# Kernel optimization log

Measured on AMD Instinct MI355X. Metric: run time of the kernel, lower is better.

## Reference

```python
import jax, jax.numpy as jnp
import numpy as np

H = 1024          # hidden_size
NH = 16           # num_attention_heads
HD = H // NH      # attention_head_size = 64
B, S = 8, 1024
LN_EPS = 1e-12


def setup_inputs() -> dict:
    key = jax.random.key(0)
    ks = jax.random.split(key, 12)
    sc = 0.02
    return {
        "input_tensor": jax.random.normal(ks[0], (B, S, H), dtype=jnp.float32),
        "attention_mask": jnp.zeros((B, S), dtype=jnp.float32),
        # LinearMem params (quantization disabled -> plain Linear, torch layout [out,in])
        "Wq": jax.random.normal(ks[1], (H, H), dtype=jnp.float32) * sc,
        "bq": jnp.zeros((H,), dtype=jnp.float32),
        "Wk": jax.random.normal(ks[2], (H, H), dtype=jnp.float32) * sc,
        "bk": jnp.zeros((H,), dtype=jnp.float32),
        "Wv": jax.random.normal(ks[3], (H, H), dtype=jnp.float32) * sc,
        "bv": jnp.zeros((H,), dtype=jnp.float32),
        "Wo": jax.random.normal(ks[4], (H, H), dtype=jnp.float32) * sc,
        "bo": jnp.zeros((H,), dtype=jnp.float32),
        "ln_gamma": jnp.ones((H,), dtype=jnp.float32),
        "ln_beta": jnp.zeros((H,), dtype=jnp.float32),
    }


def _heads(x):  # [B,S,H] -> [B,NH,S,HD]
    return x.reshape(B, S, NH, HD).transpose(0, 2, 1, 3)


def reference(input_tensor, attention_mask, Wq, bq, Wk, bk, Wv, bv, Wo, bo, ln_gamma, ln_beta):
    # Q/K/V projections (LinearMem with quantization disabled == Linear)
    q = _heads(jnp.einsum('bsh,oh->bso', input_tensor, Wq) + bq)
    k = _heads(jnp.einsum('bsh,oh->bso', input_tensor, Wk) + bk)
    v = _heads(jnp.einsum('bsh,oh->bso', input_tensor, Wv) + bv)
    scores = jnp.einsum('bnqd,bnkd->bnqk', q, k) / np.float32(np.sqrt(HD))
    scores = scores + attention_mask[:, None, None, :]  # additive mask [B,1,1,S]
    probs = jax.nn.softmax(scores, axis=-1)  # dropout = identity in eval
    ctx = jnp.einsum('bnqk,bnkd->bnqd', probs, v)
    ctx = ctx.transpose(0, 2, 1, 3).reshape(B, S, H)
    # output projection + residual LayerNorm (eps=1e-12)
    out = jnp.einsum('bsh,oh->bso', ctx, Wo) + bo
    resid = out + input_tensor
    mu = jnp.mean(resid, axis=-1, keepdims=True)
    var = jnp.mean(jnp.square(resid - mu), axis=-1, keepdims=True)
    return (resid - mu) * jax.lax.rsqrt(var + LN_EPS) * ln_gamma + ln_beta
```

## Files before the change

### kernel.cpp

```cpp
#include <hip/hip_runtime.h>

#define NHh 16

typedef unsigned short ushortT;
typedef __attribute__((ext_vector_type(8))) short short8;
typedef __attribute__((ext_vector_type(4))) float floatx4;

__device__ __forceinline__ ushortT f2bf(float x) {
    union { float f; unsigned int u; } cv; cv.f = x;
    unsigned int u = cv.u;
    unsigned int r = u + 0x7fffu + ((u >> 16) & 1u);
    return (ushortT)(r >> 16);
}

__device__ __forceinline__ unsigned pack2_trunc(float a, float b) {
    union { float f; unsigned u; } ua, ub;
    ua.f = a; ub.f = b;
    return (ub.u & 0xffff0000u) | (ua.u >> 16);
}

__device__ __forceinline__ void gload_lds16(const ushortT* g, ushortT* l) {
    __builtin_amdgcn_global_load_lds(
        (const __attribute__((address_space(1))) void*)g,
        (__attribute__((address_space(3))) void*)l, 16, 0, 0);
}

__global__ __launch_bounds__(256) void cvt_x(const float* __restrict__ in,
                                             ushortT* __restrict__ out, int n4) {
    int i = blockIdx.x * 256 + threadIdx.x;
    if (i >= n4) return;
    float4 f = ((const float4*)in)[i];
    uint2 o;
    o.x = (unsigned)f2bf(f.x) | ((unsigned)f2bf(f.y) << 16);
    o.y = (unsigned)f2bf(f.z) | ((unsigned)f2bf(f.w) << 16);
    ((uint2*)out)[i] = o;
}

__global__ __launch_bounds__(256) void cvt_w(const float* __restrict__ W0, const float* __restrict__ W1,
                                             const float* __restrict__ W2, const float* __restrict__ W3,
                                             ushortT* __restrict__ Wall, ushortT* __restrict__ Wob, int n4) {
    int z = blockIdx.y;
    const float* in = (z == 0) ? W0 : (z == 1) ? W1 : (z == 2) ? W2 : W3;
    ushortT* out = (z < 3) ? (Wall + (size_t)z * 1048576) : Wob;
    int i = blockIdx.x * 256 + threadIdx.x;
    if (i >= n4) return;
    float4 f = ((const float4*)in)[i];
    uint2 o;
    o.x = (unsigned)f2bf(f.x) | ((unsigned)f2bf(f.y) << 16);
    o.y = (unsigned)f2bf(f.z) | ((unsigned)f2bf(f.w) << 16);
    ((uint2*)out)[i] = o;
}

__global__ __launch_bounds__(512, 1) void qkv_st(
        const ushortT* __restrict__ X, const ushortT* __restrict__ Wall,
        const float* __restrict__ b0, const float* __restrict__ b1, const float* __restrict__ b2,
        ushortT* __restrict__ Qo, ushortT* __restrict__ Ko, ushortT* __restrict__ Vo) {
    __shared__ __align__(16) ushortT As[2 * 16384];
    __shared__ __align__(16) ushortT Bs[2 * 12288];

    const int l = blockIdx.x;
    const int xcd = l & 7;
    const int j = l >> 3;
    const int mg = j >> 4;
    const int nt = j & 15;
    const int arow0 = (mg * 8 + xcd) * 256;
    const int brow0 = nt * 192;

    const int tid = threadIdx.x;
    const int lane = tid & 63;
    const int w = tid >> 6;
    const int wr = w >> 2;
    const int wc = w & 3;
    const int qd = lane >> 4, ln = lane & 15;

    const ushortT* srcA[4]; const ushortT* srcB[3];
    int oA[4], oB[3];
#pragma unroll
    for (int k = 0; k < 4; k++) {
        int o = k * 8192 + tid * 16;
        int rowblk = o >> 11, ks = (o >> 10) & 1, r = (o >> 6) & 15;
        int c2 = ((o >> 4) & 3) ^ ((r >> 3) << 1);
        srcA[k] = X + (size_t)(arow0 + rowblk * 16 + r) * 1024 + ks * 32 + c2 * 8;
        oA[k] = o;
    }
#pragma unroll
    for (int k = 0; k < 3; k++) {
        int o = k * 8192 + tid * 16;
        int rowblk = o >> 11, ks = (o >> 10) & 1, r = (o >> 6) & 15;
        int c2 = ((o >> 4) & 3) ^ ((r >> 3) << 1);
        srcB[k] = Wall + (size_t)(brow0 + rowblk * 16 + r) * 1024 + ks * 32 + c2 * 8;
        oB[k] = o;
    }

    floatx4 acc[8][3];
#pragma unroll
    for (int i = 0; i < 8; i++)
#pragma unroll
        for (int jj = 0; jj < 3; jj++) acc[i][jj] = (floatx4){0.f, 0.f, 0.f, 0.f};

#pragma unroll
    for (int k = 0; k < 4; k++) { gload_lds16(srcA[k], As + oA[k] / 2); srcA[k] += 64; }
#pragma unroll
    for (int k = 0; k < 3; k++) { gload_lds16(srcB[k], Bs + oB[k] / 2); srcB[k] += 64; }
    asm volatile("s_waitcnt vmcnt(0)" ::: "memory");
    __builtin_amdgcn_s_barrier();

    const int lnc = ln * 64 + ((qd ^ ((ln >> 3) << 1)) * 16);

    for (int T = 0; T < 16; T++) {
        const char* Ab = (const char*)As + (T & 1) * 32768;
        const char* Bb = (const char*)Bs + (T & 1) * 24576;
        short8 afr[8][2], bfr[3][2];
#pragma unroll
        for (int mi = 0; mi < 8; mi++)
#pragma unroll
            for (int ks = 0; ks < 2; ks++)
                afr[mi][ks] = *(const short8*)(Ab + (wr * 8 + mi) * 2048 + ks * 1024 + lnc);
#pragma unroll
        for (int ni = 0; ni < 3; ni++)
#pragma unroll
            for (int ks = 0; ks < 2; ks++)
                bfr[ni][ks] = *(const short8*)(Bb + (wc * 3 + ni) * 2048 + ks * 1024 + lnc);
        if (T < 15) {
            char* An = (char*)As + ((T + 1) & 1) * 32768;
            char* Bn = (char*)Bs + ((T + 1) & 1) * 24576;
#pragma unroll
            for (int k = 0; k < 4; k++) { gload_lds16(srcA[k], (ushortT*)(An + oA[k])); srcA[k] += 64; }
#pragma unroll
            for (int k = 0; k < 3; k++) { gload_lds16(srcB[k], (ushortT*)(Bn + oB[k])); srcB[k] += 64; }
        }
        __builtin_amdgcn_s_barrier();
        asm volatile("s_waitcnt lgkmcnt(0)" ::: "memory");
        __builtin_amdgcn_sched_barrier(0);
        __builtin_amdgcn_s_setprio(1);
#pragma unroll
        for (int mi = 0; mi < 8; mi++)
#pragma unroll
            for (int ni = 0; ni < 3; ni++)
#pragma unroll
                for (int ks = 0; ks < 2; ks++)
                    acc[mi][ni] = __builtin_amdgcn_mfma_f32_16x16x32_bf16(
                        afr[mi][ks], bfr[ni][ks], acc[mi][ni], 0, 0, 0);
        __builtin_amdgcn_s_setprio(0);
        asm volatile("s_waitcnt vmcnt(0)" ::: "memory");
        __builtin_amdgcn_s_barrier();
    }

#pragma unroll
    for (int ni = 0; ni < 3; ni++) {
        int n = brow0 + wc * 48 + ni * 16 + ln;
        int z = n >> 10;
        int col = n & 1023;
        int h = col >> 6, d = col & 63;
        const float* bias = (z == 0) ? b0 : (z == 1) ? b1 : b2;
        float bb = bias[col];
        if (z == 2) {
#pragma unroll
            for (int mi = 0; mi < 8; mi++) {
                int m = arow0 + wr * 128 + mi * 16 + qd * 4;
                int b = m >> 10, s = m & 1023;
                ushort4 pk;
                pk.x = f2bf(acc[mi][ni][0] + bb);
                pk.y = f2bf(acc[mi][ni][1] + bb);
                pk.z = f2bf(acc[mi][ni][2] + bb);
                pk.w = f2bf(acc[mi][ni][3] + bb);
                *(ushort4*)&Vo[((size_t)(b * NHh + h) * 64 + d) * 1024 + s] = pk;
            }
        } else {
            ushortT* Out = z ? Ko : Qo;
#pragma unroll
            for (int mi = 0; mi < 8; mi++) {
#pragma unroll
                for (int r2 = 0; r2 < 4; r2++) {
                    int m = arow0 + wr * 128 + mi * 16 + qd * 4 + r2;
                    int b = m >> 10, s = m & 1023;
                    Out[(size_t)((b * NHh + h) * 1024 + s) * 64 + d] =
                        f2bf(acc[mi][ni][r2] + bb);
                }
            }
        }
    }
}

__device__ __forceinline__ void gemm_core_256x128(
        const ushortT* __restrict__ Ap, const ushortT* __restrict__ Bp,
        int arow0, int brow0, ushortT* As3, ushortT* Bs3,
        int tid, int wr, int wc, int qd, int ln, floatx4 (&acc)[4][4]) {
    const ushortT* srcA[4]; const ushortT* srcB[2];
    int oA[4], oB[2];
#pragma unroll
    for (int k = 0; k < 4; k++) {
        int o = k * 8192 + tid * 16;
        int rowblk = o >> 11, ks = (o >> 10) & 1, r = (o >> 6) & 15;
        int c2 = ((o >> 4) & 3) ^ ((r >> 3) << 1);
        srcA[k] = Ap + (size_t)(arow0 + rowblk * 16 + r) * 1024 + ks * 32 + c2 * 8;
        oA[k] = o;
    }
#pragma unroll
    for (int k = 0; k < 2; k++) {
        int o = k * 8192 + tid * 16;
        int rowblk = o >> 11, ks = (o >> 10) & 1, r = (o >> 6) & 15;
        int c2 = ((o >> 4) & 3) ^ ((r >> 3) << 1);
        srcB[k] = Bp + (size_t)(brow0 + rowblk * 16 + r) * 1024 + ks * 32 + c2 * 8;
        oB[k] = o;
    }
#pragma unroll
    for (int t = 0; t < 2; t++) {
#pragma unroll
        for (int k = 0; k < 4; k++) {
            gload_lds16(srcA[k], (ushortT*)((char*)As3 + t * 32768 + oA[k]));
            srcA[k] += 64;
        }
#pragma unroll
        for (int k = 0; k < 2; k++) {
            gload_lds16(srcB[k], (ushortT*)((char*)Bs3 + t * 16384 + oB[k]));
            srcB[k] += 64;
        }
    }
    asm volatile("s_waitcnt vmcnt(6)" ::: "memory");
    __builtin_amdgcn_s_barrier();

    const int lnc = ln * 64 + ((qd ^ ((ln >> 3) << 1)) * 16);

    int bi = 0, si = 2;
    for (int T = 0; T < 16; T++) {
        const char* Ab = (const char*)As3 + bi * 32768;
        const char* Bb = (const char*)Bs3 + bi * 16384;
        short8 afr[4][2], bfr[4][2];
#pragma unroll
        for (int mi = 0; mi < 4; mi++)
#pragma unroll
            for (int ks = 0; ks < 2; ks++)
                afr[mi][ks] = *(const short8*)(Ab + (mi * 4 + wr) * 2048 + ks * 1024 + lnc);
#pragma unroll
        for (int ni = 0; ni < 4; ni++)
#pragma unroll
            for (int ks = 0; ks < 2; ks++)
                bfr[ni][ks] = *(const short8*)(Bb + (ni * 2 + wc) * 2048 + ks * 1024 + lnc);
        if (T < 14) {
#pragma unroll
            for (int k = 0; k < 4; k++) {
                gload_lds16(srcA[k], (ushortT*)((char*)As3 + si * 32768 + oA[k]));
                srcA[k] += 64;
            }
#pragma unroll
            for (int k = 0; k < 2; k++) {
                gload_lds16(srcB[k], (ushortT*)((char*)Bs3 + si * 16384 + oB[k]));
                srcB[k] += 64;
            }
        }
        __builtin_amdgcn_s_barrier();
        asm volatile("s_waitcnt lgkmcnt(0)" ::: "memory");
        __builtin_amdgcn_sched_barrier(0);
        __builtin_amdgcn_s_setprio(1);
#pragma unroll
        for (int mi = 0; mi < 4; mi++)
#pragma unroll
            for (int ni = 0; ni < 4; ni++)
#pragma unroll
                for (int ks = 0; ks < 2; ks++)
                    acc[mi][ni] = __builtin_amdgcn_mfma_f32_16x16x32_bf16(
                        afr[mi][ks], bfr[ni][ks], acc[mi][ni], 0, 0, 0);
        __builtin_amdgcn_s_setprio(0);
        if (T < 14) { asm volatile("s_waitcnt vmcnt(6)" ::: "memory"); }
        else        { asm volatile("s_waitcnt vmcnt(0)" ::: "memory"); }
        __builtin_amdgcn_s_barrier();
        bi = (bi == 2) ? 0 : bi + 1;
        si = (si == 2) ? 0 : si + 1;
    }
}

__global__ __launch_bounds__(512, 1) void oproj_gemm3(const ushortT* __restrict__ A,
        const ushortT* __restrict__ Wt, const float* __restrict__ bias, float* __restrict__ Pj) {
    __shared__ __align__(16) ushortT As3[3 * 16384];
    __shared__ __align__(16) ushortT Bs3[3 * 8192];

    const int l = blockIdx.x;
    const int xcd = l & 7;
    const int j = l >> 3;
    const int tid = threadIdx.x;
    const int lane = tid & 63;
    const int w = tid >> 6;
    const int wr = w >> 1, wc = w & 1;
    const int qd = lane >> 4, ln = lane & 15;

    const int arow0 = ((j & 3) * 8 + xcd) * 256;
    const int brow0 = (j >> 2) * 128;

    floatx4 acc[4][4];
#pragma unroll
    for (int i = 0; i < 4; i++)
#pragma unroll
        for (int jj = 0; jj < 4; jj++) acc[i][jj] = (floatx4){0.f, 0.f, 0.f, 0.f};

    gemm_core_256x128(A, Wt, arow0, brow0, As3, Bs3, tid, wr, wc, qd, ln, acc);

#pragma unroll
    for (int ni = 0; ni < 4; ni++) {
        int n = brow0 + ni * 32 + wc * 16 + ln;
        float bb = bias[n];
#pragma unroll
        for (int mi = 0; mi < 4; mi++) {
#pragma unroll
            for (int r2 = 0; r2 < 4; r2++) {
                int m = arow0 + mi * 64 + wr * 16 + qd * 4 + r2;
                Pj[(size_t)m * 1024 + n] = acc[mi][ni][r2] + bb;
            }
        }
    }
}

__global__ __launch_bounds__(256, 2) void attn_kernel(const ushortT* __restrict__ Q,
        const ushortT* __restrict__ K, const ushortT* __restrict__ Vg_t,
        const float* __restrict__ mask, ushortT* __restrict__ ctx) {
    __shared__ __align__(16) ushortT Ks[128 * 64];
    __shared__ __align__(16) ushortT Vt[64 * 128];
    __shared__ __align__(16) ushortT Ps[4][64 * 72];

    const int tid = threadIdx.x;
    const int lane = tid & 63;
    const int w = tid >> 6;
    const int qd = lane >> 4;
    const int ln = lane & 15;
    const int l = blockIdx.x;
    const int bh = l & 127;
    const int b = bh >> 4;
    const int h = bh & 15;
    const int qb = l >> 7;

    const ushortT* Qg = Q + (size_t)bh * 65536;
    const ushortT* Kg = K + (size_t)bh * 65536;
    const ushortT* Vg = Vg_t + (size_t)bh * 65536;
    const float* mrow = mask + b * 1024;
    const float LOG2E = 1.4426950408889634f;
    const float SCL = 0.125f * 1.4426950408889634f;

    short8 qf[4][2];
#pragma unroll
    for (int nj = 0; nj < 4; nj++)
#pragma unroll
        for (int ks = 0; ks < 2; ks++)
            qf[nj][ks] = *(const short8*)(Qg + (size_t)(qb * 256 + w * 64 + nj * 16 + ln) * 64 + ks * 32 + qd * 8);

    float lst[4] = {0.f, 0.f, 0.f, 0.f};
    floatx4 accO[4][4];
#pragma unroll
    for (int i = 0; i < 4; i++)
#pragma unroll
        for (int j = 0; j < 4; j++) accO[i][j] = (floatx4){0.f, 0.f, 0.f, 0.f};

    const int ksr = lane >> 3;
    const int kc  = lane & 7;
    const int vdr = lane >> 4;
    const int vcc = lane & 15;

    for (int kt = 0; kt < 8; ++kt) {
        __syncthreads();

#pragma unroll
        for (int ii = 0; ii < 4; ii++) {
            int i = w * 4 + ii;
            int srow = i * 8 + ksr;
            gload_lds16(Kg + (size_t)(kt * 128 + srow) * 64 + (kc ^ ksr) * 8,
                        Ks + i * 512 + lane * 8);
        }
#pragma unroll
        for (int ii = 0; ii < 4; ii++) {
            int i = w * 4 + ii;
            int d = i * 4 + vdr;
            gload_lds16(Vg + (size_t)d * 1024 + kt * 128 + (vcc ^ (d & 15)) * 8,
                        Vt + i * 512 + lane * 8);
        }

        __syncthreads();

#pragma unroll
        for (int h2 = 0; h2 < 2; ++h2) {
            const int s0g = kt * 128 + h2 * 64;

#pragma unroll
            for (int njp = 0; njp < 2; ++njp) {
                floatx4 sv[4][2];
#pragma unroll
                for (int mi = 0; mi < 4; mi++)
#pragma unroll
                    for (int j = 0; j < 2; j++) sv[mi][j] = (floatx4){0.f, 0.f, 0.f, 0.f};
#pragma unroll
                for (int ks = 0; ks < 2; ks++) {
                    short8 af[4];
#pragma unroll
                    for (int mi = 0; mi < 4; mi++)
                        af[mi] = *(const short8*)&Ks[(h2 * 64 + mi * 16 + ln) * 64 +
                                                     (((ks * 4 + qd) ^ (ln & 7)) * 8)];
#pragma unroll
                    for (int mi = 0; mi < 4; mi++)
#pragma unroll
                        for (int j = 0; j < 2; j++)
                            sv[mi][j] = __builtin_amdgcn_mfma_f32_16x16x32_bf16(af[mi], qf[njp * 2 + j][ks], sv[mi][j], 0, 0, 0);
                }

                float rs0 = 0.f, rs1 = 0.f;
#pragma unroll
                for (int mi = 0; mi < 4; mi++) {
                    floatx4 m4 = *(const floatx4*)(mrow + s0g + mi * 16 + qd * 4);
                    float p00 = __builtin_amdgcn_exp2f(sv[mi][0][0] * SCL + m4[0] * LOG2E);
                    float p01 = __builtin_amdgcn_exp2f(sv[mi][0][1] * SCL + m4[1] * LOG2E);
                    float p02 = __builtin_amdgcn_exp2f(sv[mi][0][2] * SCL + m4[2] * LOG2E);
                    float p03 = __builtin_amdgcn_exp2f(sv[mi][0][3] * SCL + m4[3] * LOG2E);
                    float p10 = __builtin_amdgcn_exp2f(sv[mi][1][0] * SCL + m4[0] * LOG2E);
                    float p11 = __builtin_amdgcn_exp2f(sv[mi][1][1] * SCL + m4[1] * LOG2E);
                    float p12 = __builtin_amdgcn_exp2f(sv[mi][1][2] * SCL + m4[2] * LOG2E);
                    float p13 = __builtin_amdgcn_exp2f(sv[mi][1][3] * SCL + m4[3] * LOG2E);
                    rs0 += (p00 + p01) + (p02 + p03);
                    rs1 += (p10 + p11) + (p12 + p13);
                    uint2 w0, w1;
                    w0.x = pack2_trunc(p00, p01); w0.y = pack2_trunc(p02, p03);
                    w1.x = pack2_trunc(p10, p11); w1.y = pack2_trunc(p12, p13);
                    *(uint2*)&Ps[w][(njp * 32 + ln) * 72 + mi * 16 + qd * 4] = w0;
                    *(uint2*)&Ps[w][(njp * 32 + 16 + ln) * 72 + mi * 16 + qd * 4] = w1;
                }
                rs0 += __shfl_xor(rs0, 16, 64); rs0 += __shfl_xor(rs0, 32, 64);
                rs1 += __shfl_xor(rs1, 16, 64); rs1 += __shfl_xor(rs1, 32, 64);
                lst[njp * 2 + 0] += rs0;
                lst[njp * 2 + 1] += rs1;
            }

#pragma unroll
            for (int ks2 = 0; ks2 < 2; ks2++) {
                short8 ap[4], bv[4];
#pragma unroll
                for (int i = 0; i < 4; i++)
                    ap[i] = *(const short8*)&Ps[w][(i * 16 + ln) * 72 + ks2 * 32 + qd * 8];
#pragma unroll
                for (int j = 0; j < 4; j++)
                    bv[j] = *(const short8*)&Vt[(j * 16 + ln) * 128 +
                                                (((h2 * 8 + ks2 * 4 + qd) ^ ln) * 8)];
#pragma unroll
                for (int i = 0; i < 4; i++)
#pragma unroll
                    for (int j = 0; j < 4; j++)
                        accO[i][j] = __builtin_amdgcn_mfma_f32_16x16x32_bf16(ap[i], bv[j], accO[i][j], 0, 0, 0);
            }
        }
    }

#pragma unroll
    for (int i = 0; i < 4; i++) {
#pragma unroll
        for (int r = 0; r < 4; r++) {
            float lv = __shfl(lst[i], qd * 4 + r, 64);
            float linv = 1.f / lv;
            int q = qb * 256 + w * 64 + i * 16 + qd * 4 + r;
#pragma unroll
            for (int j = 0; j < 4; j++) {
                int d = j * 16 + ln;
                ctx[((size_t)(b * 1024 + q)) * 1024 + h * 64 + d] = f2bf(accO[i][j][r] * linv);
            }
        }
    }
}

__global__ __launch_bounds__(256) void ln_kernel(const float* __restrict__ Pj, const float* __restrict__ X,
        const float* __restrict__ gamma, const float* __restrict__ beta, float* __restrict__ out) {
    __shared__ float red[8];
    int row = blockIdx.x;
    int t = threadIdx.x;
    const float4 p4 = ((const float4*)(Pj + (size_t)row * 1024))[t];
    const float4 x4 = ((const float4*)(X + (size_t)row * 1024))[t];
    float r0 = p4.x + x4.x, r1 = p4.y + x4.y, r2 = p4.z + x4.z, r3 = p4.w + x4.w;
    float s = r0 + r1 + r2 + r3;
    float ss = r0 * r0 + r1 * r1 + r2 * r2 + r3 * r3;
#pragma unroll
    for (int o = 1; o < 64; o <<= 1) { s += __shfl_xor(s, o, 64); ss += __shfl_xor(ss, o, 64); }
    int w = t >> 6;
    if ((t & 63) == 0) { red[w] = s; red[4 + w] = ss; }
    __syncthreads();
    s = red[0] + red[1] + red[2] + red[3];
    ss = red[4] + red[5] + red[6] + red[7];
    float mu = s * (1.f / 1024.f);
    float var = ss * (1.f / 1024.f) - mu * mu;
    float inv = rsqrtf(var + 1e-12f);
    const float4 g4 = ((const float4*)gamma)[t];
    const float4 b4 = ((const float4*)beta)[t];
    float4 o4;
    o4.x = (r0 - mu) * inv * g4.x + b4.x;
    o4.y = (r1 - mu) * inv * g4.y + b4.y;
    o4.z = (r2 - mu) * inv * g4.z + b4.z;
    o4.w = (r3 - mu) * inv * g4.w + b4.w;
    ((float4*)(out + (size_t)row * 1024))[t] = o4;
}

extern "C" void kernel_launch(void* const* d_in, const int* in_sizes, int n_in,
                              void* d_out, int out_size, void* d_ws, size_t ws_size,
                              hipStream_t stream) {
    const float* x     = (const float*)d_in[0];
    const float* mask  = (const float*)d_in[1];
    const float* Wq    = (const float*)d_in[2];
    const float* bq    = (const float*)d_in[3];
    const float* Wk    = (const float*)d_in[4];
    const float* bk    = (const float*)d_in[5];
    const float* Wv    = (const float*)d_in[6];
    const float* bv    = (const float*)d_in[7];
    const float* Wo    = (const float*)d_in[8];
    const float* bo    = (const float*)d_in[9];
    const float* gamma = (const float*)d_in[10];
    const float* beta  = (const float*)d_in[11];
    float* out = (float*)d_out;

    char* ws = (char*)d_ws;
    ushortT* Xb   = (ushortT*)(ws);
    ushortT* Wall = (ushortT*)(ws + (16u << 20));
    ushortT* Wob  = (ushortT*)(ws + (22u << 20));
    ushortT* Qb   = (ushortT*)(ws + (24u << 20));
    ushortT* Kb   = (ushortT*)(ws + (40u << 20));
    ushortT* Vb   = (ushortT*)(ws + (56u << 20));
    ushortT* Cb   = (ushortT*)(ws);
    float*   Pj   = (float*)(ws + (24u << 20));

    cvt_x<<<8192, 256, 0, stream>>>(x, Xb, 2097152);
    cvt_w<<<dim3(1024, 4), 256, 0, stream>>>(Wq, Wk, Wv, Wo, Wall, Wob, 262144);
    qkv_st<<<512, 512, 0, stream>>>(Xb, Wall, bq, bk, bv, Qb, Kb, Vb);
    attn_kernel<<<512, 256, 0, stream>>>(Qb, Kb, Vb, mask, Cb);
    oproj_gemm3<<<256, 512, 0, stream>>>(Cb, Wob, bo, Pj);
    ln_kernel<<<8192, 256, 0, stream>>>(Pj, x, gamma, beta, out);
}
```

Measured before the change: 276.8 us.

## Split attention block across eight waves with 32 queries each

```diff
diff --git a/kernel.cpp b/kernel.cpp
--- a/kernel.cpp
+++ b/kernel.cpp
@@ -310,12 +310,12 @@
     }
 }
 
-__global__ __launch_bounds__(256, 2) void attn_kernel(const ushortT* __restrict__ Q,
+__global__ __launch_bounds__(512, 4) void attn8(const ushortT* __restrict__ Q,
         const ushortT* __restrict__ K, const ushortT* __restrict__ Vg_t,
         const float* __restrict__ mask, ushortT* __restrict__ ctx) {
     __shared__ __align__(16) ushortT Ks[128 * 64];
     __shared__ __align__(16) ushortT Vt[64 * 128];
-    __shared__ __align__(16) ushortT Ps[4][64 * 72];
+    __shared__ __align__(16) ushortT Ps[8][32 * 36];
 
     const int tid = threadIdx.x;
     const int lane = tid & 63;
@@ -335,19 +335,19 @@
     const float LOG2E = 1.4426950408889634f;
     const float SCL = 0.125f * 1.4426950408889634f;
 
-    short8 qf[4][2];
-#pragma unroll
-    for (int nj = 0; nj < 4; nj++)
+    short8 qf[2][2];
+#pragma unroll
+    for (int g = 0; g < 2; g++)
 #pragma unroll
         for (int ks = 0; ks < 2; ks++)
-            qf[nj][ks] = *(const short8*)(Qg + (size_t)(qb * 256 + w * 64 + nj * 16 + ln) * 64 + ks * 32 + qd * 8);
-
-    float lst[4] = {0.f, 0.f, 0.f, 0.f};
-    floatx4 accO[4][4];
-#pragma unroll
-    for (int i = 0; i < 4; i++)
-#pragma unroll
-        for (int j = 0; j < 4; j++) accO[i][j] = (floatx4){0.f, 0.f, 0.f, 0.f};
+            qf[g][ks] = *(const short8*)(Qg + (size_t)(qb * 256 + w * 32 + g * 16 + ln) * 64 + ks * 32 + qd * 8);
+
+    float lst[2] = {0.f, 0.f};
+    floatx4 accO[2][4];
+#pragma unroll
+    for (int g = 0; g < 2; g++)
+#pragma unroll
+        for (int j = 0; j < 4; j++) accO[g][j] = (floatx4){0.f, 0.f, 0.f, 0.f};
 
     const int ksr = lane >> 3;
     const int kc  = lane & 7;
@@ -358,15 +358,15 @@
         __syncthreads();
 
 #pragma unroll
-        for (int ii = 0; ii < 4; ii++) {
-            int i = w * 4 + ii;
+        for (int ii = 0; ii < 2; ii++) {
+            int i = w * 2 + ii;
             int srow = i * 8 + ksr;
             gload_lds16(Kg + (size_t)(kt * 128 + srow) * 64 + (kc ^ ksr) * 8,
                         Ks + i * 512 + lane * 8);
         }
 #pragma unroll
-        for (int ii = 0; ii < 4; ii++) {
-            int i = w * 4 + ii;
+        for (int ii = 0; ii < 2; ii++) {
+            int i = w * 2 + ii;
             int d = i * 4 + vdr;
             gload_lds16(Vg + (size_t)d * 1024 + kt * 128 + (vcc ^ (d & 15)) * 8,
                         Vt + i * 512 + lane * 8);
@@ -376,85 +376,81 @@
 
 #pragma unroll
         for (int h2 = 0; h2 < 2; ++h2) {
-            const int s0g = kt * 128 + h2 * 64;
-
-#pragma unroll
-            for (int njp = 0; njp < 2; ++njp) {
-                floatx4 sv[4][2];
-#pragma unroll
-                for (int mi = 0; mi < 4; mi++)
-#pragma unroll
-                    for (int j = 0; j < 2; j++) sv[mi][j] = (floatx4){0.f, 0.f, 0.f, 0.f};
+#pragma unroll
+            for (int mip = 0; mip < 2; ++mip) {
+                floatx4 sv[2][2];
+#pragma unroll
+                for (int mi2 = 0; mi2 < 2; mi2++)
+#pragma unroll
+                    for (int g = 0; g < 2; g++) sv[mi2][g] = (floatx4){0.f, 0.f, 0.f, 0.f};
 #pragma unroll
                 for (int ks = 0; ks < 2; ks++) {
-                    short8 af[4];
-#pragma unroll
-                    for (int mi = 0; mi < 4; mi++)
-                        af[mi] = *(const short8*)&Ks[(h2 * 64 + mi * 16 + ln) * 64 +
-                                                     (((ks * 4 + qd) ^ (ln & 7)) * 8)];
-#pragma unroll
-                    for (int mi = 0; mi < 4; mi++)
-#pragma unroll
-                        for (int j = 0; j < 2; j++)
-                            sv[mi][j] = __builtin_amdgcn_mfma_f32_16x16x32_bf16(af[mi], qf[njp * 2 + j][ks], sv[mi][j], 0, 0, 0);
+                    short8 af[2];
+#pragma unroll
+                    for (int mi2 = 0; mi2 < 2; mi2++)
+                        af[mi2] = *(const short8*)&Ks[(h2 * 64 + mip * 32 + mi2 * 16 + ln) * 64 +
+                                                      (((ks * 4 + qd) ^ (ln & 7)) * 8)];
+#pragma unroll
+                    for (int mi2 = 0; mi2 < 2; mi2++)
+#pragma unroll
+                        for (int g = 0; g < 2; g++)
+                            sv[mi2][g] = __builtin_amdgcn_mfma_f32_16x16x32_bf16(af[mi2], qf[g][ks], sv[mi2][g], 0, 0, 0);
                 }
 
-                float rs0 = 0.f, rs1 = 0.f;
-#pragma unroll
-                for (int mi = 0; mi < 4; mi++) {
-                    floatx4 m4 = *(const floatx4*)(mrow + s0g + mi * 16 + qd * 4);
-                    float p00 = __builtin_amdgcn_exp2f(sv[mi][0][0] * SCL + m4[0] * LOG2E);
-                    float p01 = __builtin_amdgcn_exp2f(sv[mi][0][1] * SCL + m4[1] * LOG2E);
-                    float p02 = __builtin_amdgcn_exp2f(sv[mi][0][2] * SCL + m4[2] * LOG2E);
-                    float p03 = __builtin_amdgcn_exp2f(sv[mi][0][3] * SCL + m4[3] * LOG2E);
-                    float p10 = __builtin_amdgcn_exp2f(sv[mi][1][0] * SCL + m4[0] * LOG2E);
-                    float p11 = __builtin_amdgcn_exp2f(sv[mi][1][1] * SCL + m4[1] * LOG2E);
-                    float p12 = __builtin_amdgcn_exp2f(sv[mi][1][2] * SCL + m4[2] * LOG2E);
-                    float p13 = __builtin_amdgcn_exp2f(sv[mi][1][3] * SCL + m4[3] * LOG2E);
-                    rs0 += (p00 + p01) + (p02 + p03);
-                    rs1 += (p10 + p11) + (p12 + p13);
-                    uint2 w0, w1;
-                    w0.x = pack2_trunc(p00, p01); w0.y = pack2_trunc(p02, p03);
-                    w1.x = pack2_trunc(p10, p11); w1.y = pack2_trunc(p12, p13);
-                    *(uint2*)&Ps[w][(njp * 32 + ln) * 72 + mi * 16 + qd * 4] = w0;
-                    *(uint2*)&Ps[w][(njp * 32 + 16 + ln) * 72 + mi * 16 + qd * 4] = w1;
+#pragma unroll
+                for (int mi2 = 0; mi2 < 2; mi2++) {
+                    floatx4 m4 = *(const floatx4*)(mrow + kt * 128 + h2 * 64 + mip * 32 + mi2 * 16 + qd * 4);
+                    floatx4 mm;
+                    mm[0] = m4[0] * LOG2E; mm[1] = m4[1] * LOG2E;
+                    mm[2] = m4[2] * LOG2E; mm[3] = m4[3] * LOG2E;
+#pragma unroll
+                    for (int g = 0; g < 2; g++) {
+                        float p0 = __builtin_amdgcn_exp2f(sv[mi2][g][0] * SCL + mm[0]);
+                        float p1 = __builtin_amdgcn_exp2f(sv[mi2][g][1] * SCL + mm[1]);
+                        float p2 = __builtin_amdgcn_exp2f(sv[mi2][g][2] * SCL + mm[2]);
+                        float p3 = __builtin_amdgcn_exp2f(sv[mi2][g][3] * SCL + mm[3]);
+                        lst[g] += (p0 + p1) + (p2 + p3);
+                        uint2 wv;
+                        wv.x = pack2_trunc(p0, p1);
+                        wv.y = pack2_trunc(p2, p3);
+                        *(uint2*)&Ps[w][(g * 16 + ln) * 36 + mi2 * 16 + qd * 4] = wv;
+                    }
                 }
-                rs0 += __shfl_xor(rs0, 16, 64); rs0 += __shfl_xor(rs0, 32, 64);
-                rs1 += __shfl_xor(rs1, 16, 64); rs1 += __shfl_xor(rs1, 32, 64);
-                lst[njp * 2 + 0] += rs0;
-                lst[njp * 2 + 1] += rs1;
-            }
-
-#pragma unroll
-            for (int ks2 = 0; ks2 < 2; ks2++) {
-                short8 ap[4], bv[4];
-#pragma unroll
-                for (int i = 0; i < 4; i++)
-                    ap[i] = *(const short8*)&Ps[w][(i * 16 + ln) * 72 + ks2 * 32 + qd * 8];
+
+                short8 ap[2], bv[4];
+#pragma unroll
+                for (int g = 0; g < 2; g++)
+                    ap[g] = *(const short8*)&Ps[w][(g * 16 + ln) * 36 + qd * 8];
 #pragma unroll
                 for (int j = 0; j < 4; j++)
                     bv[j] = *(const short8*)&Vt[(j * 16 + ln) * 128 +
-                                                (((h2 * 8 + ks2 * 4 + qd) ^ ln) * 8)];
-#pragma unroll
-                for (int i = 0; i < 4; i++)
+                                                (((h2 * 8 + mip * 4 + qd) ^ ln) * 8)];
+#pragma unroll
+                for (int g = 0; g < 2; g++)
 #pragma unroll
                     for (int j = 0; j < 4; j++)
-                        accO[i][j] = __builtin_amdgcn_mfma_f32_16x16x32_bf16(ap[i], bv[j], accO[i][j], 0, 0, 0);
-            }
-        }
-    }
-
-#pragma unroll
-    for (int i = 0; i < 4; i++) {
+                        accO[g][j] = __builtin_amdgcn_mfma_f32_16x16x32_bf16(ap[g], bv[j], accO[g][j], 0, 0, 0);
+            }
+        }
+    }
+
+#pragma unroll
+    for (int g = 0; g < 2; g++) {
+        lst[g] += __shfl_xor(lst[g], 16, 64);
+        lst[g] += __shfl_xor(lst[g], 32, 64);
+    }
+
+#pragma unroll
+    for (int g = 0; g < 2; g++) {
 #pragma unroll
         for (int r = 0; r < 4; r++) {
-            float lv = __shfl(lst[i], qd * 4 + r, 64);
+            float lv = __shfl(lst[g], qd * 4 + r, 64);
             float linv = 1.f / lv;
-            int q = qb * 256 + w * 64 + i * 16 + qd * 4 + r;
+            int q = qb * 256 + w * 32 + g * 16 + qd * 4 + r;
 #pragma unroll
             for (int j = 0; j < 4; j++) {
                 int d = j * 16 + ln;
-                ctx[((size_t)(b * 1024 + q)) * 1024 + h * 64 + d] = f2bf(accO[i][j][r] * linv);
+                ctx[((size_t)(b * 1024 + q)) * 1024 + h * 64 + d] = f2bf(accO[g][j][r] * linv);
             }
         }
     }
@@ -520,7 +516,7 @@
     cvt_x<<<8192, 256, 0, stream>>>(x, Xb, 2097152);
     cvt_w<<<dim3(1024, 4), 256, 0, stream>>>(Wq, Wk, Wv, Wo, Wall, Wob, 262144);
     qkv_st<<<512, 512, 0, stream>>>(Xb, Wall, bq, bk, bv, Qb, Kb, Vb);
-    attn_kernel<<<512, 256, 0, stream>>>(Qb, Kb, Vb, mask, Cb);
+    attn8<<<512, 512, 0, stream>>>(Qb, Kb, Vb, mask, Cb);
     oproj_gemm3<<<256, 512, 0, stream>>>(Cb, Wob, bo, Pj);
     ln_kernel<<<8192, 256, 0, stream>>>(Pj, x, gamma, beta, out);
 }
```

After: 262.1 us. 1.06x faster.
